# Kernel tuning notes

Hardware: AMD Instinct MI355X
Metric: run time of the kernel (lower is better)

The kernel has to match this reference:

```python
import jax, jax.numpy as jnp
import numpy as np

EPS = 0.05
N_ITER = 50
IN_DIM = 4096
PROJ_DIM = 128
BATCH = 4096


def sinkhorn_loss(x, y, eps=EPS, n_iter=N_ITER):
    # x, y: [B, N, D]
    B, N, _ = x.shape
    # squared euclidean cost, matches torch.cdist(p=2).pow(2): [B, N, N]
    C = jnp.sum((x[:, :, None, :] - y[:, None, :, :]) ** 2, axis=-1)
    log_K = -C / eps
    log_ab = -jnp.log(jnp.asarray(N, x.dtype))  # log_a = log_b = -log N
    log_u0 = jnp.zeros((B, N), x.dtype)
    log_v0 = jnp.zeros((B, N), x.dtype)

    def step(carry, _):
        log_u, log_v = carry
        log_u = log_ab - jax.scipy.special.logsumexp(log_K + log_v[:, None, :], axis=-1)
        log_v = log_ab - jax.scipy.special.logsumexp(log_K + log_u[:, :, None], axis=-2)
        return (log_u, log_v), None

    (log_u, log_v), _ = jax.lax.scan(step, (log_u0, log_v0), None, length=n_iter)
    log_T = log_K + log_u[:, :, None] + log_v[:, None, :]
    T = jnp.exp(log_T)
    transport_cost = jnp.sum(T * C, axis=(1, 2))
    entropic = eps * jnp.sum(T * (log_T - 1.0), axis=(1, 2))
    return jnp.mean(transport_cost + entropic)


def setup_inputs() -> dict:
    key = jax.random.key(0)
    ks = jax.random.split(key, 6)
    scale = 1.0 / np.sqrt(IN_DIM)
    return {
        "x_ct": jax.random.normal(ks[0], (BATCH, IN_DIM), jnp.float32),
        "x_txt": jax.random.normal(ks[1], (BATCH, IN_DIM), jnp.float32),
        "x_lab": jax.random.normal(ks[2], (BATCH, IN_DIM), jnp.float32),
        "W_ct": jax.random.uniform(ks[3], (PROJ_DIM, IN_DIM), jnp.float32, -scale, scale),
        "W_txt": jax.random.uniform(ks[4], (PROJ_DIM, IN_DIM), jnp.float32, -scale, scale),
        "W_lab": jax.random.uniform(ks[5], (PROJ_DIM, IN_DIM), jnp.float32, -scale, scale),
    }


def reference(x_ct, x_txt, x_lab, W_ct, W_txt, W_lab):
    # Linear projections (no bias): z = x @ W.T -> [B, P]
    z_ct = x_ct @ W_ct.T
    z_txt = x_txt @ W_txt.T
    z_lab = x_lab @ W_lab.T
    # unsqueeze(1): each becomes a point cloud of N=1 points
    z_ct_e = z_ct[:, None, :]
    z_txt_e = z_txt[:, None, :]
    z_lab_e = z_lab[:, None, :]
    loss_ct_txt = sinkhorn_loss(z_ct_e, z_txt_e)
    loss_ct_lab = sinkhorn_loss(z_ct_e, z_lab_e)
    loss_txt_lab = sinkhorn_loss(z_txt_e, z_lab_e)
    ot_loss = (loss_ct_txt + loss_ct_lab + loss_txt_lab) / 3.0
    aligned = (z_ct + z_txt + z_lab) / 3.0
    return (aligned, ot_loss)
```

## Files before the change

kernel.cpp:

```cpp
#include <hip/hip_runtime.h>
#include <stdint.h>

typedef __attribute__((ext_vector_type(8))) short short8;
typedef __attribute__((ext_vector_type(4))) float f32x4;

#define K_DIM 4096
#define N_DIM 128
#define M_DIM 4096
#define MN ((size_t)M_DIM * N_DIM)

__device__ __forceinline__ uint16_t f2bf(float f) {
    uint32_t u = __float_as_uint(f);
    return (uint16_t)((u + 0x7FFFu + ((u >> 16) & 1u)) >> 16);
}

__device__ __forceinline__ short8 cvt8(const float4 lo, const float4 hi) {
    short8 r;
    r[0] = (short)f2bf(lo.x); r[1] = (short)f2bf(lo.y);
    r[2] = (short)f2bf(lo.z); r[3] = (short)f2bf(lo.w);
    r[4] = (short)f2bf(hi.x); r[5] = (short)f2bf(hi.y);
    r[6] = (short)f2bf(hi.z); r[7] = (short)f2bf(hi.w);
    return r;
}

__global__ __launch_bounds__(256) void prep_kernel(
    const float* __restrict__ W0, const float* __restrict__ W1,
    const float* __restrict__ W2, uint16_t* __restrict__ Wb)
{
    int gid = blockIdx.x * 256 + threadIdx.x;
    int g = gid >> 16;
    int e = (gid & 65535) * 8;
    const float* W = (g == 0) ? W0 : (g == 1) ? W1 : W2;
    float4 lo = *(const float4*)(W + e);
    float4 hi = *(const float4*)(W + e + 4);
    *(short8*)(Wb + (size_t)g * (N_DIM * K_DIM) + e) = cvt8(lo, hi);
}

template<int NS>
__global__ __launch_bounds__(256) void gemm3_kernel(
    const float* __restrict__ x0, const float* __restrict__ x1,
    const float* __restrict__ x2, const uint16_t* __restrict__ Wb,
    float* __restrict__ zpart)
{
    __shared__ uint16_t lds[2][8192];

    const int tid  = threadIdx.x;
    const int lane = tid & 63;
    const int wv   = tid >> 6;

    const int per = (192 * NS) >> 3;
    const int lid = (blockIdx.x & 7) * per + (blockIdx.x >> 3);
    const int g   = lid / (NS * 64);
    const int rem = lid % (NS * 64);
    const int ks  = rem >> 6;
    const int mt  = rem & 63;
    const int k0  = ks * (K_DIM / NS);
    const int NT  = (K_DIM / NS) / 64;

    const float* x = (g == 0) ? x0 : (g == 1) ? x1 : x2;
    const uint16_t* Wg = Wb + (size_t)g * (N_DIM * K_DIM);
    float* zp = zpart + (size_t)(ks * 3 + g) * MN;

    const int c16 = lane & 15;
    const int qg  = lane >> 4;
    const int rowbase = mt * 64 + wv * 16;
    const float* aptr = x + (size_t)(rowbase + c16) * K_DIM + qg * 8 + k0;

    const int t8 = tid >> 3, slot = tid & 7;
    const uint16_t* wsrc[4];
#pragma unroll
    for (int c = 0; c < 4; ++c) {
        int col = c * 32 + t8;
        wsrc[c] = Wg + (size_t)col * K_DIM + (slot ^ (col & 7)) * 8 + k0;
    }

    f32x4 acc[8];
#pragma unroll
    for (int nf = 0; nf < 8; ++nf) acc[nf] = (f32x4)0.f;

    auto stage = [&](int p, int kbase) {
#pragma unroll
        for (int c = 0; c < 4; ++c) {
            __builtin_amdgcn_global_load_lds(
                (const __attribute__((address_space(1))) uint32_t*)(wsrc[c] + kbase),
                (__attribute__((address_space(3))) uint32_t*)&lds[p][c * 2048 + wv * 512],
                16, 0, 0);
        }
    };

    stage(0, 0);
    float4 a_cur[4], a_nxt[4];
    a_cur[0] = *(const float4*)(aptr);
    a_cur[1] = *(const float4*)(aptr + 4);
    a_cur[2] = *(const float4*)(aptr + 32);
    a_cur[3] = *(const float4*)(aptr + 36);

    int p = 0;
    for (int kt = 0; kt < NT; ++kt) {
        const int kbase = kt * 64;
        __syncthreads();
        if (kt + 1 < NT) {
            stage(p ^ 1, kbase + 64);
            const float* ap = aptr + kbase + 64;
            a_nxt[0] = *(const float4*)(ap);
            a_nxt[1] = *(const float4*)(ap + 4);
            a_nxt[2] = *(const float4*)(ap + 32);
            a_nxt[3] = *(const float4*)(ap + 36);
        }
#pragma unroll
        for (int h = 0; h < 2; ++h) {
            short8 af = cvt8(a_cur[2 * h], a_cur[2 * h + 1]);
            const int boff = c16 * 64 + (((h * 4) + qg) ^ (lane & 7)) * 8;
#pragma unroll
            for (int nf = 0; nf < 8; ++nf) {
                short8 bf = *(const short8*)&lds[p][nf * 1024 + boff];
                acc[nf] = __builtin_amdgcn_mfma_f32_16x16x32_bf16(af, bf, acc[nf], 0, 0, 0);
            }
        }
#pragma unroll
        for (int i = 0; i < 4; ++i) a_cur[i] = a_nxt[i];
        p ^= 1;
    }

#pragma unroll
    for (int nf = 0; nf < 8; ++nf) {
#pragma unroll
        for (int r = 0; r < 4; ++r) {
            zp[(size_t)(rowbase + qg * 4 + r) * N_DIM + nf * 16 + c16] = acc[nf][r];
        }
    }
}

template<int NS>
__global__ __launch_bounds__(256) void combine_kernel(
    const float* __restrict__ zpart, float* __restrict__ out,
    float* __restrict__ partials)
{
    const int tid = threadIdx.x;
    const size_t i = ((size_t)blockIdx.x * 256 + tid) * 4;

    float4 zsum[3];
#pragma unroll
    for (int g = 0; g < 3; ++g) {
        float4 s = *(const float4*)(zpart + (size_t)g * MN + i);
#pragma unroll
        for (int ks = 1; ks < NS; ++ks) {
            const float4 v = *(const float4*)(zpart + (size_t)(ks * 3 + g) * MN + i);
            s.x += v.x; s.y += v.y; s.z += v.z; s.w += v.w;
        }
        zsum[g] = s;
    }
    const float4 a = zsum[0], b = zsum[1], c = zsum[2];
    float4 al;
    al.x = (a.x + b.x + c.x) * (1.f / 3.f);
    al.y = (a.y + b.y + c.y) * (1.f / 3.f);
    al.z = (a.z + b.z + c.z) * (1.f / 3.f);
    al.w = (a.w + b.w + c.w) * (1.f / 3.f);
    *(float4*)(out + i) = al;

    float s = 0.f;
#define LOSS(u, v, w) { float d1 = (u)-(v), d2 = (u)-(w), d3 = (v)-(w); s += d1*d1 + d2*d2 + d3*d3; }
    LOSS(a.x, b.x, c.x) LOSS(a.y, b.y, c.y) LOSS(a.z, b.z, c.z) LOSS(a.w, b.w, c.w)
#undef LOSS
#pragma unroll
    for (int off = 32; off > 0; off >>= 1) s += __shfl_xor(s, off);
    __shared__ float wsum[4];
    if ((tid & 63) == 0) wsum[tid >> 6] = s;
    __syncthreads();
    if (tid == 0) partials[blockIdx.x] = wsum[0] + wsum[1] + wsum[2] + wsum[3];
}

__global__ __launch_bounds__(256) void finalize_kernel(
    const float* __restrict__ partials, float* __restrict__ out)
{
    const int tid = threadIdx.x;
    float s = partials[tid] + partials[tid + 256];
#pragma unroll
    for (int off = 32; off > 0; off >>= 1) s += __shfl_xor(s, off);
    __shared__ float wsum[4];
    if ((tid & 63) == 0) wsum[tid >> 6] = s;
    __syncthreads();
    if (tid == 0)
        out[MN] = (wsum[0] + wsum[1] + wsum[2] + wsum[3]) * (1.f / 12288.f) - 0.05f;
}

extern "C" void kernel_launch(void* const* d_in, const int* in_sizes, int n_in,
                              void* d_out, int out_size, void* d_ws, size_t ws_size,
                              hipStream_t stream)
{
    const float* x0 = (const float*)d_in[0];
    const float* x1 = (const float*)d_in[1];
    const float* x2 = (const float*)d_in[2];
    const float* W0 = (const float*)d_in[3];
    const float* W1 = (const float*)d_in[4];
    const float* W2 = (const float*)d_in[5];
    float* out = (float*)d_out;

    const size_t zpart4_bytes = (size_t)4 * 3 * MN * sizeof(float);
    const size_t wb_bytes = (size_t)3 * N_DIM * K_DIM * sizeof(uint16_t);
    const bool split4 = ws_size >= zpart4_bytes + wb_bytes + 2048;

    char* ws = (char*)d_ws;
    float*    zpart    = (float*)ws;
    size_t    zbytes   = split4 ? zpart4_bytes : (size_t)3 * MN * sizeof(float);
    uint16_t* Wb       = (uint16_t*)(ws + zbytes);
    float*    partials = (float*)(ws + zbytes + wb_bytes);

    prep_kernel<<<768, 256, 0, stream>>>(W0, W1, W2, Wb);
    if (split4) {
        gemm3_kernel<4><<<768, 256, 0, stream>>>(x0, x1, x2, Wb, zpart);
        combine_kernel<4><<<512, 256, 0, stream>>>(zpart, out, partials);
    } else {
        gemm3_kernel<1><<<192, 256, 0, stream>>>(x0, x1, x2, Wb, zpart);
        combine_kernel<1><<<512, 256, 0, stream>>>(zpart, out, partials);
    }
    finalize_kernel<<<1, 256, 0, stream>>>(partials, out);
}
```

Before: 52.52 us.

## Split-K by eight with bf16 fragment-layout partials and layout-aware combine

```diff
diff --git a/kernel.cpp b/kernel.cpp
--- a/kernel.cpp
+++ b/kernel.cpp
@@ -3,15 +3,21 @@
 
 typedef __attribute__((ext_vector_type(8))) short short8;
 typedef __attribute__((ext_vector_type(4))) float f32x4;
+typedef __attribute__((ext_vector_type(4))) uint32_t u32x4;
 
 #define K_DIM 4096
 #define N_DIM 128
 #define M_DIM 4096
 #define MN ((size_t)M_DIM * N_DIM)
+#define NS 8
+#define FRAG_PER_SLAB ((size_t)64 * 8192)
 
 __device__ __forceinline__ uint16_t f2bf(float f) {
     uint32_t u = __float_as_uint(f);
     return (uint16_t)((u + 0x7FFFu + ((u >> 16) & 1u)) >> 16);
+}
+__device__ __forceinline__ float bf2f(uint16_t h) {
+    return __uint_as_float((uint32_t)h << 16);
 }
 
 __device__ __forceinline__ short8 cvt8(const float4 lo, const float4 hi) {
@@ -36,11 +42,10 @@
     *(short8*)(Wb + (size_t)g * (N_DIM * K_DIM) + e) = cvt8(lo, hi);
 }
 
-template<int NS>
 __global__ __launch_bounds__(256) void gemm3_kernel(
     const float* __restrict__ x0, const float* __restrict__ x1,
     const float* __restrict__ x2, const uint16_t* __restrict__ Wb,
-    float* __restrict__ zpart)
+    uint16_t* __restrict__ zpart)
 {
     __shared__ uint16_t lds[2][8192];
 
@@ -59,7 +64,6 @@
 
     const float* x = (g == 0) ? x0 : (g == 1) ? x1 : x2;
     const uint16_t* Wg = Wb + (size_t)g * (N_DIM * K_DIM);
-    float* zp = zpart + (size_t)(ks * 3 + g) * MN;
 
     const int c16 = lane & 15;
     const int qg  = lane >> 4;
@@ -122,46 +126,65 @@
         p ^= 1;
     }
 
+    uint32_t dw[16];
 #pragma unroll
     for (int nf = 0; nf < 8; ++nf) {
-#pragma unroll
-        for (int r = 0; r < 4; ++r) {
-            zp[(size_t)(rowbase + qg * 4 + r) * N_DIM + nf * 16 + c16] = acc[nf][r];
-        }
-    }
-}
-
-template<int NS>
+        dw[nf * 2]     = (uint32_t)f2bf(acc[nf][0]) | ((uint32_t)f2bf(acc[nf][1]) << 16);
+        dw[nf * 2 + 1] = (uint32_t)f2bf(acc[nf][2]) | ((uint32_t)f2bf(acc[nf][3]) << 16);
+    }
+    uint16_t* zp = zpart + (size_t)(ks * 3 + g) * FRAG_PER_SLAB
+                 + (size_t)mt * 8192 + (size_t)(wv * 64 + lane) * 32;
+    uint32_t* zp32 = (uint32_t*)zp;
+#pragma unroll
+    for (int j = 0; j < 4; ++j) {
+        u32x4 v = { dw[j * 4], dw[j * 4 + 1], dw[j * 4 + 2], dw[j * 4 + 3] };
+        *(u32x4*)(zp32 + j * 4) = v;
+    }
+}
+
 __global__ __launch_bounds__(256) void combine_kernel(
-    const float* __restrict__ zpart, float* __restrict__ out,
+    const uint16_t* __restrict__ zpart, float* __restrict__ out,
     float* __restrict__ partials)
 {
-    const int tid = threadIdx.x;
-    const size_t i = ((size_t)blockIdx.x * 256 + tid) * 4;
-
-    float4 zsum[3];
-#pragma unroll
-    for (int g = 0; g < 3; ++g) {
-        float4 s = *(const float4*)(zpart + (size_t)g * MN + i);
-#pragma unroll
-        for (int ks = 1; ks < NS; ++ks) {
-            const float4 v = *(const float4*)(zpart + (size_t)(ks * 3 + g) * MN + i);
-            s.x += v.x; s.y += v.y; s.z += v.z; s.w += v.w;
-        }
-        zsum[g] = s;
-    }
-    const float4 a = zsum[0], b = zsum[1], c = zsum[2];
-    float4 al;
-    al.x = (a.x + b.x + c.x) * (1.f / 3.f);
-    al.y = (a.y + b.y + c.y) * (1.f / 3.f);
-    al.z = (a.z + b.z + c.z) * (1.f / 3.f);
-    al.w = (a.w + b.w + c.w) * (1.f / 3.f);
-    *(float4*)(out + i) = al;
+    const int tid  = threadIdx.x;
+    const int gtid = blockIdx.x * 256 + tid;
+    const size_t F0 = (size_t)gtid * 8;
+
+    const int idx_base = (int)(F0 & 31);
+    const int lane = (int)((F0 >> 5) & 63);
+    const int wv   = (int)((F0 >> 11) & 3);
+    const int mt   = (int)(F0 >> 13);
+    const int c16  = lane & 15;
+    const int qg   = lane >> 4;
+    const int rowb = mt * 64 + wv * 16 + qg * 4;
+
+    float zs[3][8];
+#pragma unroll
+    for (int g = 0; g < 3; ++g)
+#pragma unroll
+        for (int v = 0; v < 8; ++v) zs[g][v] = 0.f;
+
+#pragma unroll
+    for (int ks = 0; ks < NS; ++ks) {
+#pragma unroll
+        for (int g = 0; g < 3; ++g) {
+            const short8 pv = *(const short8*)(zpart + (size_t)(ks * 3 + g) * FRAG_PER_SLAB + F0);
+#pragma unroll
+            for (int v = 0; v < 8; ++v) zs[g][v] += bf2f((uint16_t)pv[v]);
+        }
+    }
 
     float s = 0.f;
-#define LOSS(u, v, w) { float d1 = (u)-(v), d2 = (u)-(w), d3 = (v)-(w); s += d1*d1 + d2*d2 + d3*d3; }
-    LOSS(a.x, b.x, c.x) LOSS(a.y, b.y, c.y) LOSS(a.z, b.z, c.z) LOSS(a.w, b.w, c.w)
-#undef LOSS
+#pragma unroll
+    for (int v = 0; v < 8; ++v) {
+        const float a = zs[0][v], b = zs[1][v], c = zs[2][v];
+        const int idx = idx_base + v;
+        const int nf = idx >> 2, r = idx & 3;
+        out[(size_t)(rowb + r) * N_DIM + nf * 16 + c16] = (a + b + c) * (1.f / 3.f);
+        const float d1 = a - b, d2 = a - c, d3 = b - c;
+        s += d1 * d1 + d2 * d2 + d3 * d3;
+    }
+
 #pragma unroll
     for (int off = 32; off > 0; off >>= 1) s += __shfl_xor(s, off);
     __shared__ float wsum[4];
@@ -174,7 +197,7 @@
     const float* __restrict__ partials, float* __restrict__ out)
 {
     const int tid = threadIdx.x;
-    float s = partials[tid] + partials[tid + 256];
+    float s = partials[tid];
 #pragma unroll
     for (int off = 32; off > 0; off >>= 1) s += __shfl_xor(s, off);
     __shared__ float wsum[4];
@@ -196,23 +219,16 @@
     const float* W2 = (const float*)d_in[5];
     float* out = (float*)d_out;
 
-    const size_t zpart4_bytes = (size_t)4 * 3 * MN * sizeof(float);
-    const size_t wb_bytes = (size_t)3 * N_DIM * K_DIM * sizeof(uint16_t);
-    const bool split4 = ws_size >= zpart4_bytes + wb_bytes + 2048;
+    const size_t zpart_bytes = (size_t)NS * 3 * FRAG_PER_SLAB * sizeof(uint16_t);
+    const size_t wb_bytes    = (size_t)3 * N_DIM * K_DIM * sizeof(uint16_t);
 
     char* ws = (char*)d_ws;
-    float*    zpart    = (float*)ws;
-    size_t    zbytes   = split4 ? zpart4_bytes : (size_t)3 * MN * sizeof(float);
-    uint16_t* Wb       = (uint16_t*)(ws + zbytes);
-    float*    partials = (float*)(ws + zbytes + wb_bytes);
-
-    prep_kernel<<<768, 256, 0, stream>>>(W0, W1, W2, Wb);
-    if (split4) {
-        gemm3_kernel<4><<<768, 256, 0, stream>>>(x0, x1, x2, Wb, zpart);
-        combine_kernel<4><<<512, 256, 0, stream>>>(zpart, out, partials);
-    } else {
-        gemm3_kernel<1><<<192, 256, 0, stream>>>(x0, x1, x2, Wb, zpart);
-        combine_kernel<1><<<512, 256, 0, stream>>>(zpart, out, partials);
-    }
-    finalize_kernel<<<1, 256, 0, stream>>>(partials, out);
-}
+    uint16_t* zpart    = (uint16_t*)ws;
+    uint16_t* Wb       = (uint16_t*)(ws + zpart_bytes);
+    float*    partials = (float*)(ws + zpart_bytes + wb_bytes);
+
+    prep_kernel    <<< 768, 256, 0, stream>>>(W0, W1, W2, Wb);
+    gemm3_kernel   <<<1536, 256, 0, stream>>>(x0, x1, x2, Wb, zpart);
+    combine_kernel <<< 256, 256, 0, stream>>>(zpart, out, partials);
+    finalize_kernel<<<   1, 256, 0, stream>>>(partials, out);
+}
```

After: 54.85 us. +4.4%, slower.
